# Performance work log

Measured on AMD Instinct MI355X. Metric: run time of the kernel, lower is better.

The kernel has to match this reference:

```python
import jax, jax.numpy as jnp
import numpy as np

HEADS = 8
DIM_HEAD = 64
BN_EPS = 1e-5

def setup_inputs() -> dict:
    key = jax.random.key(0)
    ks = jax.random.split(key, 6)
    B, N, D = 8, 1024, 512
    inner = HEADS * DIM_HEAD  # 512
    return {
        "x": jax.random.normal(ks[0], (B, N, D), dtype=jnp.float32),
        "w_qkv": jax.random.normal(ks[1], (D, 3 * inner), dtype=jnp.float32) * (D ** -0.5),
        "conv_w": jax.random.normal(ks[2], (HEADS, HEADS), dtype=jnp.float32) * (HEADS ** -0.5),
        "conv_b": jax.random.normal(ks[3], (HEADS,), dtype=jnp.float32) * 0.02,
        "bn_gamma": jnp.ones((HEADS,), dtype=jnp.float32),
        "bn_beta": jnp.zeros((HEADS,), dtype=jnp.float32),
        "w_out": jax.random.normal(ks[4], (inner, D), dtype=jnp.float32) * (inner ** -0.5),
        "b_out": jnp.zeros((D,), dtype=jnp.float32),
    }

def reference(x, w_qkv, conv_w, conv_b, bn_gamma, bn_beta, w_out, b_out):
    B, N, D = x.shape
    H, dh = HEADS, DIM_HEAD
    scale = dh ** -0.5
    qkv = x @ w_qkv  # [B, N, 3*H*dh]
    q, k, v = jnp.split(qkv, 3, axis=-1)
    # b n (h d) -> b h n d
    q = q.reshape(B, N, H, dh).transpose(0, 2, 1, 3)
    k = k.reshape(B, N, H, dh).transpose(0, 2, 1, 3)
    v = v.reshape(B, N, H, dh).transpose(0, 2, 1, 3)
    attn = jnp.einsum('bhnd,bhmd->bhnm', q, k) * scale
    attn = jax.nn.softmax(attn, axis=-1)
    # 1x1 conv across heads (channels = heads)
    attn = jnp.einsum('gh,bhnm->bgnm', conv_w, attn) + conv_b[None, :, None, None]
    # BatchNorm2d in training mode: batch stats over (B, N, N) per head, biased variance
    mean = attn.mean(axis=(0, 2, 3), keepdims=True)
    var = attn.var(axis=(0, 2, 3), keepdims=True)
    attn = (attn - mean) * jax.lax.rsqrt(var + BN_EPS)
    attn = attn * bn_gamma[None, :, None, None] + bn_beta[None, :, None, None]
    # reatten_scale = 1.0 (transform_scale=False)
    out = jnp.einsum('bhnm,bhmd->bhnd', attn, v)
    out = out.transpose(0, 2, 1, 3).reshape(B, N, H * dh)  # b h n d -> b n (h d)
    return out @ w_out + b_out
```

## Files before the change

kernel.cpp:

```cpp
#include <hip/hip_runtime.h>
#include <math.h>


#define Bz 8
#define Nn 1024
#define Dd 512
#define Hh 8
#define DH 64
#define INNER 512
#define QW 1536
#define SCALE 0.125f
#define BN_EPS 1e-5f

typedef _Float16 __f16;
typedef __f16 f16x8 __attribute__((ext_vector_type(8)));
typedef float f32x4 __attribute__((ext_vector_type(4)));

#define MFMA16(a, b, c) __builtin_amdgcn_mfma_f32_16x16x32_f16((a), (b), (c), 0, 0, 0)

__device__ __forceinline__ unsigned short f2h(float f) {
  union { __f16 h; unsigned short s; } v;
  v.h = (__f16)f;
  return v.s;
}
__device__ __forceinline__ float h2f(unsigned short s) {
  union { unsigned short s; __f16 h; } v;
  v.s = s;
  return (float)v.h;
}

#define WB_XB 0u
#define WB_QKV 8388608u
#define WB_VT 33554432u
#define WB_O1 41943040u
#define WB_O1BF 58720256u
#define WB_WQT 67108864u
#define WB_WOT 68681728u
#define WB_RINV 69206016u
#define WB_VSUM 69468160u
#define WB_STATS 69484544u
#define WB_AC 69484608u

__global__ __launch_bounds__(256) void k_xbf(const float* __restrict__ X,
                                             unsigned short* __restrict__ XB) {
  const size_t i = ((size_t)blockIdx.x * 256 + threadIdx.x) * 8;
  float4 f0 = *(const float4*)(X + i);
  float4 f1 = *(const float4*)(X + i + 4);
  unsigned short o[8] = {f2h(f0.x), f2h(f0.y), f2h(f0.z), f2h(f0.w),
                         f2h(f1.x), f2h(f1.y), f2h(f1.z), f2h(f1.w)};
  *(uint4*)(XB + i) = *(uint4*)o;
}

__global__ __launch_bounds__(256) void k_transpose(const float* __restrict__ src,
                                                   unsigned short* __restrict__ dst,
                                                   int R, int C) {
  __shared__ float tile[32][33];
  const int tc = blockIdx.x * 32, tr = blockIdx.y * 32;
  const int lx = threadIdx.x & 31, ly = threadIdx.x >> 5;
#pragma unroll
  for (int i = 0; i < 32; i += 8)
    tile[ly + i][lx] = src[(size_t)(tr + ly + i) * C + tc + lx];
  __syncthreads();
#pragma unroll
  for (int i = 0; i < 32; i += 8)
    dst[(size_t)(tc + ly + i) * R + tr + lx] = f2h(tile[lx][ly + i]);
}

__global__ __launch_bounds__(256) void k_qkv(const unsigned short* __restrict__ XB,
                                             const unsigned short* __restrict__ WQT,
                                             unsigned short* __restrict__ qkv,
                                             unsigned short* __restrict__ vT) {
  extern __shared__ char smem[];
  unsigned short(*sA)[40] = (unsigned short(*)[40])smem;
  unsigned short(*sB)[40] = (unsigned short(*)[40])(smem + 128 * 40 * 2);
  unsigned short* sEp = (unsigned short*)smem;
  const int t = threadIdx.x;
  const int col0 = blockIdx.x * 128;
  const int row0 = blockIdx.y * 128;
  const bool isqk = (col0 < 2 * INNER);
  const int l = t & 63, w = t >> 6;
  const int wm = (w & 1) * 64, wn = (w >> 1) * 64;
  const int lm = l & 15, lq = l >> 4;
  const int srow = t >> 1, skc = (t & 1) * 16;
  f32x4 acc[4][4] = {};
  for (int k0 = 0; k0 < Dd; k0 += 32) {
    {
      const unsigned short* src = XB + (size_t)(row0 + srow) * Dd + k0 + skc;
      *(uint4*)&sA[srow][skc] = *(const uint4*)src;
      *(uint4*)&sA[srow][skc + 8] = *(const uint4*)(src + 8);
    }
    {
      const unsigned short* srcB = WQT + (size_t)(col0 + srow) * Dd + k0 + skc;
      *(uint4*)&sB[srow][skc] = *(const uint4*)srcB;
      *(uint4*)&sB[srow][skc + 8] = *(const uint4*)(srcB + 8);
    }
    __syncthreads();
    f16x8 af[4], bfr[4];
#pragma unroll
    for (int i = 0; i < 4; i++) af[i] = *(const f16x8*)&sA[wm + 16 * i + lm][lq * 8];
#pragma unroll
    for (int j = 0; j < 4; j++) bfr[j] = *(const f16x8*)&sB[wn + 16 * j + lm][lq * 8];
    if (isqk) {
#pragma unroll
      for (int i = 0; i < 4; i++)
#pragma unroll
        for (int j = 0; j < 4; j++) acc[i][j] = MFMA16(bfr[i], af[j], acc[i][j]);
    } else {
#pragma unroll
      for (int i = 0; i < 4; i++)
#pragma unroll
        for (int j = 0; j < 4; j++) acc[i][j] = MFMA16(af[i], bfr[j], acc[i][j]);
    }
    __syncthreads();
  }
  if (isqk) {
#pragma unroll
    for (int jc = 0; jc < 4; jc++)
#pragma unroll
      for (int ir = 0; ir < 4; ir++) {
        unsigned short us[4];
#pragma unroll
        for (int r = 0; r < 4; r++) us[r] = f2h(acc[jc][ir][r]);
        *(uint2*)&sEp[(wm + 16 * ir + lm) * 136 + wn + 16 * jc + 4 * lq] = *(uint2*)us;
      }
    __syncthreads();
    const int row = t >> 1, half = t & 1;
    const unsigned short* src = &sEp[row * 136 + half * 64];
    unsigned short* dst = qkv + (size_t)(row0 + row) * QW + col0 + half * 64;
#pragma unroll
    for (int c = 0; c < 8; c++) *(uint4*)(dst + c * 8) = *(const uint4*)(src + c * 8);
  } else {
#pragma unroll
    for (int ir = 0; ir < 4; ir++)
#pragma unroll
      for (int jc = 0; jc < 4; jc++) {
        unsigned short us[4];
#pragma unroll
        for (int r = 0; r < 4; r++) us[r] = f2h(acc[ir][jc][r]);
        *(uint2*)&sEp[(wn + 16 * jc + lm) * 136 + wm + 16 * ir + 4 * lq] = *(uint2*)us;
      }
    __syncthreads();
    const int row = t >> 1, half = t & 1;
    const int gd = col0 - 2 * INNER + row;
    const int bq = row0 >> 10, mseq0 = row0 & 1023;
    const unsigned short* src = &sEp[row * 136 + half * 64];
    unsigned short* dst =
        vT + (((size_t)(bq * Hh + (gd >> 6)) * DH + (gd & 63)) << 10) + mseq0 + half * 64;
#pragma unroll
    for (int c = 0; c < 8; c++) *(uint4*)(dst + c * 8) = *(const uint4*)(src + c * 8);
  }
}

__global__ __launch_bounds__(256) void k_vsum(const unsigned short* __restrict__ vT,
                                              float* __restrict__ vsum) {
  const int bg = blockIdx.x;
  const int d = threadIdx.x >> 2, qq = threadIdx.x & 3;
  __shared__ float red[64][4];
  const unsigned short* p = vT + ((size_t)bg * DH + d) * Nn + qq * 256;
  float s = 0.f;
  for (int m = 0; m < 256; m += 4) {
    uint2 rr = *(const uint2*)(p + m);
    s += h2f((unsigned short)(rr.x & 0xffff)) + h2f((unsigned short)(rr.x >> 16)) +
         h2f((unsigned short)(rr.y & 0xffff)) + h2f((unsigned short)(rr.y >> 16));
  }
  red[d][qq] = s;
  __syncthreads();
  if (threadIdx.x < 64)
    vsum[(size_t)bg * DH + threadIdx.x] =
        red[threadIdx.x][0] + red[threadIdx.x][1] + red[threadIdx.x][2] + red[threadIdx.x][3];
}

__global__ __launch_bounds__(512, 2) void k_rsum(const unsigned short* __restrict__ qkv,
                                                 float* __restrict__ rinv) {
  const int b = blockIdx.x;
  const int n0 = blockIdx.y * 16;
  const int t = threadIdx.x;
  const int w = t >> 6, l = t & 63;
  const int lm = l & 15, lq = l >> 4;
  f16x8 qf[2];
  {
    const unsigned short* qp = qkv + (size_t)(b * Nn + n0 + lm) * QW + w * DH + lq * 8;
    qf[0] = *(const f16x8*)qp;
    qf[1] = *(const f16x8*)(qp + 32);
  }
  float psum[4] = {};
  for (int m0 = 0; m0 < Nn; m0 += 32) {
#pragma unroll
    for (int jm = 0; jm < 2; jm++) {
      const unsigned short* kp =
          qkv + (size_t)(b * Nn + m0 + 16 * jm + lm) * QW + INNER + w * DH + lq * 8;
      f16x8 k0 = *(const f16x8*)kp;
      f16x8 k1 = *(const f16x8*)(kp + 32);
      f32x4 lac = {};
      lac = MFMA16(qf[0], k0, lac);
      lac = MFMA16(qf[1], k1, lac);
#pragma unroll
      for (int r = 0; r < 4; r++) psum[r] += __expf(lac[r] * SCALE);
    }
  }
#pragma unroll
  for (int r = 0; r < 4; r++) {
    float s = psum[r];
    s += __shfl_xor(s, 1);
    s += __shfl_xor(s, 2);
    s += __shfl_xor(s, 4);
    s += __shfl_xor(s, 8);
    if (lm == 0) rinv[(size_t)(b * Hh + w) * Nn + n0 + lq * 4 + r] = 1.0f / s;
  }
}

__global__ __launch_bounds__(512, 2) void k_fuse(const unsigned short* __restrict__ qkv,
                                                 const unsigned short* __restrict__ vT,
                                                 const float* __restrict__ rinv,
                                                 const float* __restrict__ conv_w,
                                                 float* __restrict__ O1,
                                                 float* __restrict__ stats) {
  __shared__ __align__(16) unsigned short sS[8][16][36];
  __shared__ __align__(16) unsigned short sU[8][16][40];
  __shared__ float sRed[8][16];
  const int b = blockIdx.x;
  const int n0 = blockIdx.y * 16;
  const int t = threadIdx.x;
  const int w = t >> 6, l = t & 63;
  const int lm = l & 15, lq = l >> 4;
  const int mxn = t >> 5, mxm = t & 31;
  float cw[64];
#pragma unroll
  for (int i = 0; i < 64; i++) cw[i] = conv_w[i];
  f16x8 qf[2];
  {
    const unsigned short* qp = qkv + (size_t)(b * Nn + n0 + lm) * QW + w * DH + lq * 8;
    qf[0] = *(const f16x8*)qp;
    qf[1] = *(const f16x8*)(qp + 32);
  }
  float rv[4];
#pragma unroll
  for (int r = 0; r < 4; r++)
    rv[r] = rinv[(size_t)(b * Hh + w) * Nn + n0 + lq * 4 + r];
  f32x4 oacc[4] = {};
  float su[8] = {}, su2[8] = {};
  for (int m0 = 0; m0 < Nn; m0 += 32) {
    {
#pragma unroll
      for (int jm = 0; jm < 2; jm++) {
        const unsigned short* kp =
            qkv + (size_t)(b * Nn + m0 + 16 * jm + lm) * QW + INNER + w * DH + lq * 8;
        f16x8 k0 = *(const f16x8*)kp;
        f16x8 k1 = *(const f16x8*)(kp + 32);
        f32x4 lac = {};
        lac = MFMA16(qf[0], k0, lac);
        lac = MFMA16(qf[1], k1, lac);
#pragma unroll
        for (int r = 0; r < 4; r++)
          sS[w][lq * 4 + r][16 * jm + lm] = f2h(__expf(lac[r] * SCALE) * rv[r]);
      }
    }
    __syncthreads();
    {
      float sv[8];
#pragma unroll
      for (int h = 0; h < 8; h++) sv[h] = h2f(sS[h][mxn][mxm]);
#pragma unroll
      for (int g = 0; g < 8; g++) {
        float u = 0.f;
#pragma unroll
        for (int h = 0; h < 8; h++) u += cw[g * 8 + h] * sv[h];
        su[g] += u;
        su2[g] += u * u;
        sU[g][mxn][mxm] = f2h(u);
      }
    }
    __syncthreads();
    {
      f16x8 uf = *(const f16x8*)&sU[w][lm][lq * 8];
#pragma unroll
      for (int j = 0; j < 4; j++) {
        const unsigned short* vp =
            vT + (((size_t)(b * Hh + w) * DH + 16 * j + lm) << 10) + m0 + lq * 8;
        f16x8 vv = *(const f16x8*)vp;
        oacc[j] = MFMA16(uf, vv, oacc[j]);
      }
    }
  }
#pragma unroll
  for (int j = 0; j < 4; j++)
#pragma unroll
    for (int r = 0; r < 4; r++)
      O1[((size_t)(b * Hh + w) * Nn + n0 + lq * 4 + r) * DH + 16 * j + lm] = oacc[j][r];
#pragma unroll
  for (int g = 0; g < 8; g++) {
    float a = su[g], q = su2[g];
    for (int off = 32; off; off >>= 1) {
      a += __shfl_down(a, off);
      q += __shfl_down(q, off);
    }
    if (l == 0) {
      sRed[w][g] = a;
      sRed[w][8 + g] = q;
    }
  }
  __syncthreads();
  if (t < 16) {
    float s = 0.f;
#pragma unroll
    for (int ww = 0; ww < 8; ww++) s += sRed[ww][t];
    atomicAdd(&stats[t], s);
  }
}

__global__ void k_alpha(const float* __restrict__ stats, const float* __restrict__ bn_gamma,
                        const float* __restrict__ bn_beta, float* __restrict__ ac) {
  const int g = threadIdx.x;
  if (g < 8) {
    const float cnt = (float)Bz * (float)Nn * (float)Nn;
    float Eu = stats[g] / cnt;
    float Eu2 = stats[8 + g] / cnt;
    float inv = rsqrtf(Eu2 - Eu * Eu + BN_EPS);
    float alpha = bn_gamma[g] * inv;
    ac[g] = alpha;
    ac[8 + g] = bn_beta[g] - Eu * alpha;
  }
}

__global__ __launch_bounds__(256) void k_o1aff(const float* __restrict__ O1,
                                               const float* __restrict__ vsum,
                                               const float* __restrict__ ac,
                                               unsigned short* __restrict__ O1BF) {
  const size_t i4 = ((size_t)blockIdx.x * 256 + threadIdx.x) * 4;
  const int bg = (int)(i4 >> 16);
  const int g = bg & 7;
  const int d = (int)(i4 & 63);
  float4 a = *(const float4*)(O1 + i4);
  float4 v = *(const float4*)(vsum + (size_t)bg * DH + d);
  const float al = ac[g], cc = ac[8 + g];
  unsigned short o[4] = {f2h(al * a.x + cc * v.x), f2h(al * a.y + cc * v.y),
                         f2h(al * a.z + cc * v.z), f2h(al * a.w + cc * v.w)};
  *(uint2*)(O1BF + i4) = *(uint2*)o;
}

__global__ __launch_bounds__(256) void k_out(const unsigned short* __restrict__ O1BF,
                                             const unsigned short* __restrict__ WOT,
                                             const float* __restrict__ bout,
                                             float* __restrict__ out) {
  __shared__ unsigned short sA[128][40];
  __shared__ unsigned short sB[128][40];
  const int t = threadIdx.x;
  const int col0 = blockIdx.x * 128, row0 = blockIdx.y * 128;
  const int l = t & 63, w = t >> 6;
  const int wm = (w & 1) * 64, wn = (w >> 1) * 64;
  const int lm = l & 15, lq = l >> 4;
  const int srow = t >> 1, skc = (t & 1) * 16;
  const int b = row0 >> 10;
  const int nn = (row0 + srow) & 1023;
  f32x4 acc[4][4] = {};
  for (int k0 = 0; k0 < INNER; k0 += 32) {
    {
      const int k = k0 + skc;
      const int g = k >> 6, dd = k & 63;
      const unsigned short* src = O1BF + ((size_t)(b * Hh + g) * Nn + nn) * DH + dd;
      *(uint4*)&sA[srow][skc] = *(const uint4*)src;
      *(uint4*)&sA[srow][skc + 8] = *(const uint4*)(src + 8);
    }
    {
      const unsigned short* srcB = WOT + (size_t)(col0 + srow) * INNER + k0 + skc;
      *(uint4*)&sB[srow][skc] = *(const uint4*)srcB;
      *(uint4*)&sB[srow][skc + 8] = *(const uint4*)(srcB + 8);
    }
    __syncthreads();
    f16x8 af[4], bfr[4];
#pragma unroll
    for (int i = 0; i < 4; i++) af[i] = *(const f16x8*)&sA[wm + 16 * i + lm][lq * 8];
#pragma unroll
    for (int j = 0; j < 4; j++) bfr[j] = *(const f16x8*)&sB[wn + 16 * j + lm][lq * 8];
#pragma unroll
    for (int i = 0; i < 4; i++)
#pragma unroll
      for (int j = 0; j < 4; j++) acc[i][j] = MFMA16(af[i], bfr[j], acc[i][j]);
    __syncthreads();
  }
#pragma unroll
  for (int j = 0; j < 4; j++) {
    const int col = col0 + wn + 16 * j + lm;
    const float bo = bout[col];
#pragma unroll
    for (int i = 0; i < 4; i++) {
      const int rbase = row0 + wm + 16 * i + lq * 4;
#pragma unroll
      for (int r = 0; r < 4; r++) out[(size_t)(rbase + r) * Dd + col] = acc[i][j][r] + bo;
    }
  }
}

extern "C" void kernel_launch(void* const* d_in, const int* in_sizes, int n_in,
                              void* d_out, int out_size, void* d_ws, size_t ws_size,
                              hipStream_t stream) {
  const float* x = (const float*)d_in[0];
  const float* w_qkv = (const float*)d_in[1];
  const float* conv_w = (const float*)d_in[2];
  const float* bn_gamma = (const float*)d_in[4];
  const float* bn_beta = (const float*)d_in[5];
  const float* w_out = (const float*)d_in[6];
  const float* b_out = (const float*)d_in[7];
  char* ws = (char*)d_ws;
  unsigned short* XB = (unsigned short*)(ws + WB_XB);
  unsigned short* QKV = (unsigned short*)(ws + WB_QKV);
  unsigned short* VT = (unsigned short*)(ws + WB_VT);
  unsigned short* WQT = (unsigned short*)(ws + WB_WQT);
  unsigned short* WOT = (unsigned short*)(ws + WB_WOT);
  float* O1 = (float*)(ws + WB_O1);
  unsigned short* O1BF = (unsigned short*)(ws + WB_O1BF);
  float* RINV = (float*)(ws + WB_RINV);
  float* VSUM = (float*)(ws + WB_VSUM);
  float* STATS = (float*)(ws + WB_STATS);
  float* AC = (float*)(ws + WB_AC);

  hipMemsetAsync(STATS, 0, 64, stream);
  k_xbf<<<2048, 256, 0, stream>>>(x, XB);
  k_transpose<<<dim3(48, 16), 256, 0, stream>>>(w_qkv, WQT, 512, 1536);
  k_transpose<<<dim3(16, 16), 256, 0, stream>>>(w_out, WOT, 512, 512);
  k_qkv<<<dim3(12, 64), 256, 34816, stream>>>(XB, WQT, QKV, VT);
  k_vsum<<<64, 256, 0, stream>>>(VT, VSUM);
  k_rsum<<<dim3(8, 64), 512, 0, stream>>>(QKV, RINV);
  k_fuse<<<dim3(8, 64), 512, 0, stream>>>(QKV, VT, RINV, conv_w, O1, STATS);
  k_alpha<<<1, 64, 0, stream>>>(STATS, bn_gamma, bn_beta, AC);
  k_o1aff<<<4096, 256, 0, stream>>>(O1, VSUM, AC, O1BF);
  k_out<<<dim3(4, 64), 256, 0, stream>>>(O1BF, WOT, b_out, (float*)d_out);
}
```

Baseline: 337.6 us.

## Keep head-mixing conv in registers via transposed MFMA; split key range across blocks

The fused attention kernel now computes scores with K as the MFMA A operand, so each lane holds all 8 heads for the same query/key positions. This lets the 1x1 head-mixing conv happen entirely in registers, removing the shared-memory staging and both __syncthreads per tile. The key dimension is split into two halves across grid z, with partial outputs summed in k_o1aff. The BN mean is now computed analytically from the conv weights, since each softmax row sums to one, which drops the first-moment reduction. The row-sum kernel is restructured the same way. The costs are higher register pressure (16 Q fragments plus 64 accumulators), an extra output buffer, and more atomics on the stats.

```diff
diff --git a/kernel.cpp b/kernel.cpp
--- a/kernel.cpp
+++ b/kernel.cpp
@@ -14,9 +14,11 @@
 
 typedef _Float16 __f16;
 typedef __f16 f16x8 __attribute__((ext_vector_type(8)));
+typedef __f16 f16x4 __attribute__((ext_vector_type(4)));
 typedef float f32x4 __attribute__((ext_vector_type(4)));
 
 #define MFMA16(a, b, c) __builtin_amdgcn_mfma_f32_16x16x32_f16((a), (b), (c), 0, 0, 0)
+#define MFMA16K16(a, b, c) __builtin_amdgcn_mfma_f32_16x16x16f16((a), (b), (c), 0, 0, 0)
 
 __device__ __forceinline__ unsigned short f2h(float f) {
   union { __f16 h; unsigned short s; } v;
@@ -32,14 +34,15 @@
 #define WB_XB 0u
 #define WB_QKV 8388608u
 #define WB_VT 33554432u
-#define WB_O1 41943040u
-#define WB_O1BF 58720256u
-#define WB_WQT 67108864u
-#define WB_WOT 68681728u
-#define WB_RINV 69206016u
-#define WB_VSUM 69468160u
-#define WB_STATS 69484544u
-#define WB_AC 69484608u
+#define WB_O1A 41943040u
+#define WB_O1B 58720256u
+#define WB_O1BF 75497472u
+#define WB_WQT 83886080u
+#define WB_WOT 85458944u
+#define WB_RINV 85983232u
+#define WB_VSUM 86245376u
+#define WB_STATS 86261760u
+#define WB_AC 86261824u
 
 __global__ __launch_bounds__(256) void k_xbf(const float* __restrict__ X,
                                              unsigned short* __restrict__ XB) {
@@ -170,151 +173,150 @@
         red[threadIdx.x][0] + red[threadIdx.x][1] + red[threadIdx.x][2] + red[threadIdx.x][3];
 }
 
-__global__ __launch_bounds__(512, 2) void k_rsum(const unsigned short* __restrict__ qkv,
+__global__ __launch_bounds__(512, 4) void k_rsum(const unsigned short* __restrict__ qkv,
                                                  float* __restrict__ rinv) {
+  __shared__ float sRed[8][8][16];
   const int b = blockIdx.x;
   const int n0 = blockIdx.y * 16;
   const int t = threadIdx.x;
   const int w = t >> 6, l = t & 63;
   const int lm = l & 15, lq = l >> 4;
-  f16x8 qf[2];
-  {
-    const unsigned short* qp = qkv + (size_t)(b * Nn + n0 + lm) * QW + w * DH + lq * 8;
-    qf[0] = *(const f16x8*)qp;
-    qf[1] = *(const f16x8*)(qp + 32);
-  }
-  float psum[4] = {};
-  for (int m0 = 0; m0 < Nn; m0 += 32) {
-#pragma unroll
-    for (int jm = 0; jm < 2; jm++) {
-      const unsigned short* kp =
-          qkv + (size_t)(b * Nn + m0 + 16 * jm + lm) * QW + INNER + w * DH + lq * 8;
-      f16x8 k0 = *(const f16x8*)kp;
-      f16x8 k1 = *(const f16x8*)(kp + 32);
+  f16x8 qf[8][2];
+#pragma unroll
+  for (int h = 0; h < 8; h++) {
+    const unsigned short* qp = qkv + (size_t)(b * Nn + n0 + lm) * QW + h * DH + lq * 8;
+    qf[h][0] = *(const f16x8*)qp;
+    qf[h][1] = *(const f16x8*)(qp + 32);
+  }
+  float psum[8] = {};
+  for (int it = 0; it < 8; it++) {
+    const int m0 = w * 16 + it * 128;
+    const unsigned short* kbase = qkv + (size_t)(b * Nn + m0 + lm) * QW + INNER + lq * 8;
+#pragma unroll
+    for (int h = 0; h < 8; h++) {
+      f16x8 k0 = *(const f16x8*)(kbase + h * DH);
+      f16x8 k1 = *(const f16x8*)(kbase + h * DH + 32);
       f32x4 lac = {};
-      lac = MFMA16(qf[0], k0, lac);
-      lac = MFMA16(qf[1], k1, lac);
-#pragma unroll
-      for (int r = 0; r < 4; r++) psum[r] += __expf(lac[r] * SCALE);
-    }
-  }
-#pragma unroll
-  for (int r = 0; r < 4; r++) {
-    float s = psum[r];
-    s += __shfl_xor(s, 1);
-    s += __shfl_xor(s, 2);
-    s += __shfl_xor(s, 4);
-    s += __shfl_xor(s, 8);
-    if (lm == 0) rinv[(size_t)(b * Hh + w) * Nn + n0 + lq * 4 + r] = 1.0f / s;
-  }
-}
-
-__global__ __launch_bounds__(512, 2) void k_fuse(const unsigned short* __restrict__ qkv,
+      lac = MFMA16(k0, qf[h][0], lac);
+      lac = MFMA16(k1, qf[h][1], lac);
+#pragma unroll
+      for (int r = 0; r < 4; r++) psum[h] += __expf(lac[r] * SCALE);
+    }
+  }
+#pragma unroll
+  for (int h = 0; h < 8; h++) {
+    float p = psum[h];
+    p += __shfl_xor(p, 16);
+    p += __shfl_xor(p, 32);
+    if (lq == 0) sRed[w][h][lm] = p;
+  }
+  __syncthreads();
+  if (t < 128) {
+    const int h = t >> 4, n = t & 15;
+    float s = 0.f;
+#pragma unroll
+    for (int ww = 0; ww < 8; ww++) s += sRed[ww][h][n];
+    rinv[(size_t)(b * Hh + h) * Nn + n0 + n] = 1.0f / s;
+  }
+}
+
+__global__ __launch_bounds__(128, 2) void k_fuse(const unsigned short* __restrict__ qkv,
                                                  const unsigned short* __restrict__ vT,
                                                  const float* __restrict__ rinv,
                                                  const float* __restrict__ conv_w,
-                                                 float* __restrict__ O1,
+                                                 float* __restrict__ O1A,
+                                                 float* __restrict__ O1B,
                                                  float* __restrict__ stats) {
-  __shared__ __align__(16) unsigned short sS[8][16][36];
-  __shared__ __align__(16) unsigned short sU[8][16][40];
-  __shared__ float sRed[8][16];
   const int b = blockIdx.x;
   const int n0 = blockIdx.y * 16;
+  const int ms = blockIdx.z;
+  float* __restrict__ O1 = ms ? O1B : O1A;
   const int t = threadIdx.x;
-  const int w = t >> 6, l = t & 63;
-  const int lm = l & 15, lq = l >> 4;
-  const int mxn = t >> 5, mxm = t & 31;
-  float cw[64];
-#pragma unroll
-  for (int i = 0; i < 64; i++) cw[i] = conv_w[i];
-  f16x8 qf[2];
-  {
-    const unsigned short* qp = qkv + (size_t)(b * Nn + n0 + lm) * QW + w * DH + lq * 8;
-    qf[0] = *(const f16x8*)qp;
-    qf[1] = *(const f16x8*)(qp + 32);
-  }
-  float rv[4];
-#pragma unroll
-  for (int r = 0; r < 4; r++)
-    rv[r] = rinv[(size_t)(b * Hh + w) * Nn + n0 + lq * 4 + r];
-  f32x4 oacc[4] = {};
-  float su[8] = {}, su2[8] = {};
-  for (int m0 = 0; m0 < Nn; m0 += 32) {
-    {
-#pragma unroll
-      for (int jm = 0; jm < 2; jm++) {
-        const unsigned short* kp =
-            qkv + (size_t)(b * Nn + m0 + 16 * jm + lm) * QW + INNER + w * DH + lq * 8;
-        f16x8 k0 = *(const f16x8*)kp;
-        f16x8 k1 = *(const f16x8*)(kp + 32);
-        f32x4 lac = {};
-        lac = MFMA16(qf[0], k0, lac);
-        lac = MFMA16(qf[1], k1, lac);
-#pragma unroll
-        for (int r = 0; r < 4; r++)
-          sS[w][lq * 4 + r][16 * jm + lm] = f2h(__expf(lac[r] * SCALE) * rv[r]);
+  const int l = t & 63, lm = l & 15, lq = l >> 4;
+  const int ghu = __builtin_amdgcn_readfirstlane(t >> 6);
+  float cw[32];
+  if (ghu == 0) {
+#pragma unroll
+    for (int i = 0; i < 32; i++) cw[i] = conv_w[i];
+  } else {
+#pragma unroll
+    for (int i = 0; i < 32; i++) cw[i] = conv_w[32 + i];
+  }
+  float rv[8];
+#pragma unroll
+  for (int h = 0; h < 8; h++) rv[h] = rinv[(size_t)(b * Hh + h) * Nn + n0 + lm];
+  f16x8 qf[8][2];
+#pragma unroll
+  for (int h = 0; h < 8; h++) {
+    const unsigned short* qp = qkv + (size_t)(b * Nn + n0 + lm) * QW + h * DH + lq * 8;
+    qf[h][0] = *(const f16x8*)qp;
+    qf[h][1] = *(const f16x8*)(qp + 32);
+  }
+  f32x4 acc[4][4] = {};
+  float su2[4] = {};
+  for (int it = 0; it < 32; it++) {
+    const int m0 = ms * 512 + it * 16;
+    const unsigned short* kbase = qkv + (size_t)(b * Nn + m0 + lm) * QW + INNER + lq * 8;
+    float u[4][4] = {};
+#pragma unroll
+    for (int h = 0; h < 8; h++) {
+      f16x8 k0 = *(const f16x8*)(kbase + h * DH);
+      f16x8 k1 = *(const f16x8*)(kbase + h * DH + 32);
+      f32x4 lac = {};
+      lac = MFMA16(k0, qf[h][0], lac);
+      lac = MFMA16(k1, qf[h][1], lac);
+      float s[4];
+#pragma unroll
+      for (int r = 0; r < 4; r++) s[r] = __expf(lac[r] * SCALE) * rv[h];
+#pragma unroll
+      for (int gl = 0; gl < 4; gl++)
+#pragma unroll
+        for (int r = 0; r < 4; r++) u[gl][r] += cw[gl * 8 + h] * s[r];
+    }
+#pragma unroll
+    for (int gl = 0; gl < 4; gl++) {
+      su2[gl] += u[gl][0] * u[gl][0] + u[gl][1] * u[gl][1] + u[gl][2] * u[gl][2] +
+                 u[gl][3] * u[gl][3];
+      f16x4 up = {(__f16)u[gl][0], (__f16)u[gl][1], (__f16)u[gl][2], (__f16)u[gl][3]};
+      const int g = ghu * 4 + gl;
+      const unsigned short* vb =
+          vT + (((size_t)(b * Hh + g) * DH + lm) << 10) + m0 + lq * 4;
+#pragma unroll
+      for (int dt = 0; dt < 4; dt++) {
+        f16x4 vf = *(const f16x4*)(vb + ((size_t)dt << 14));
+        acc[gl][dt] = MFMA16K16(up, vf, acc[gl][dt]);
       }
     }
-    __syncthreads();
-    {
-      float sv[8];
-#pragma unroll
-      for (int h = 0; h < 8; h++) sv[h] = h2f(sS[h][mxn][mxm]);
-#pragma unroll
-      for (int g = 0; g < 8; g++) {
-        float u = 0.f;
-#pragma unroll
-        for (int h = 0; h < 8; h++) u += cw[g * 8 + h] * sv[h];
-        su[g] += u;
-        su2[g] += u * u;
-        sU[g][mxn][mxm] = f2h(u);
-      }
-    }
-    __syncthreads();
-    {
-      f16x8 uf = *(const f16x8*)&sU[w][lm][lq * 8];
-#pragma unroll
-      for (int j = 0; j < 4; j++) {
-        const unsigned short* vp =
-            vT + (((size_t)(b * Hh + w) * DH + 16 * j + lm) << 10) + m0 + lq * 8;
-        f16x8 vv = *(const f16x8*)vp;
-        oacc[j] = MFMA16(uf, vv, oacc[j]);
-      }
-    }
-  }
-#pragma unroll
-  for (int j = 0; j < 4; j++)
-#pragma unroll
-    for (int r = 0; r < 4; r++)
-      O1[((size_t)(b * Hh + w) * Nn + n0 + lq * 4 + r) * DH + 16 * j + lm] = oacc[j][r];
-#pragma unroll
-  for (int g = 0; g < 8; g++) {
-    float a = su[g], q = su2[g];
-    for (int off = 32; off; off >>= 1) {
-      a += __shfl_down(a, off);
-      q += __shfl_down(q, off);
-    }
-    if (l == 0) {
-      sRed[w][g] = a;
-      sRed[w][8 + g] = q;
-    }
-  }
-  __syncthreads();
-  if (t < 16) {
-    float s = 0.f;
-#pragma unroll
-    for (int ww = 0; ww < 8; ww++) s += sRed[ww][t];
-    atomicAdd(&stats[t], s);
-  }
-}
-
-__global__ void k_alpha(const float* __restrict__ stats, const float* __restrict__ bn_gamma,
+  }
+#pragma unroll
+  for (int gl = 0; gl < 4; gl++) {
+    const int g = ghu * 4 + gl;
+#pragma unroll
+    for (int dt = 0; dt < 4; dt++)
+#pragma unroll
+      for (int r = 0; r < 4; r++)
+        O1[((size_t)(b * Hh + g) * Nn + n0 + lq * 4 + r) * DH + dt * 16 + lm] =
+            acc[gl][dt][r];
+  }
+#pragma unroll
+  for (int gl = 0; gl < 4; gl++) {
+    float q = su2[gl];
+    for (int off = 32; off; off >>= 1) q += __shfl_down(q, off);
+    if (l == 0) atomicAdd(&stats[ghu * 4 + gl], q);
+  }
+}
+
+__global__ void k_alpha(const float* __restrict__ stats, const float* __restrict__ conv_w,
+                        const float* __restrict__ bn_gamma,
                         const float* __restrict__ bn_beta, float* __restrict__ ac) {
   const int g = threadIdx.x;
   if (g < 8) {
+    float csum = 0.f;
+#pragma unroll
+    for (int h = 0; h < 8; h++) csum += conv_w[g * 8 + h];
+    const float Eu = csum / (float)Nn;
     const float cnt = (float)Bz * (float)Nn * (float)Nn;
-    float Eu = stats[g] / cnt;
-    float Eu2 = stats[8 + g] / cnt;
+    float Eu2 = stats[g] / cnt;
     float inv = rsqrtf(Eu2 - Eu * Eu + BN_EPS);
     float alpha = bn_gamma[g] * inv;
     ac[g] = alpha;
@@ -322,7 +324,8 @@
   }
 }
 
-__global__ __launch_bounds__(256) void k_o1aff(const float* __restrict__ O1,
+__global__ __launch_bounds__(256) void k_o1aff(const float* __restrict__ O1A,
+                                               const float* __restrict__ O1B,
                                                const float* __restrict__ vsum,
                                                const float* __restrict__ ac,
                                                unsigned short* __restrict__ O1BF) {
@@ -330,11 +333,12 @@
   const int bg = (int)(i4 >> 16);
   const int g = bg & 7;
   const int d = (int)(i4 & 63);
-  float4 a = *(const float4*)(O1 + i4);
+  float4 a = *(const float4*)(O1A + i4);
+  float4 bb = *(const float4*)(O1B + i4);
   float4 v = *(const float4*)(vsum + (size_t)bg * DH + d);
   const float al = ac[g], cc = ac[8 + g];
-  unsigned short o[4] = {f2h(al * a.x + cc * v.x), f2h(al * a.y + cc * v.y),
-                         f2h(al * a.z + cc * v.z), f2h(al * a.w + cc * v.w)};
+  unsigned short o[4] = {f2h(al * (a.x + bb.x) + cc * v.x), f2h(al * (a.y + bb.y) + cc * v.y),
+                         f2h(al * (a.z + bb.z) + cc * v.z), f2h(al * (a.w + bb.w) + cc * v.w)};
   *(uint2*)(O1BF + i4) = *(uint2*)o;
 }
 
@@ -407,7 +411,8 @@
   unsigned short* VT = (unsigned short*)(ws + WB_VT);
   unsigned short* WQT = (unsigned short*)(ws + WB_WQT);
   unsigned short* WOT = (unsigned short*)(ws + WB_WOT);
-  float* O1 = (float*)(ws + WB_O1);
+  float* O1Ap = (float*)(ws + WB_O1A);
+  float* O1Bp = (float*)(ws + WB_O1B);
   unsigned short* O1BF = (unsigned short*)(ws + WB_O1BF);
   float* RINV = (float*)(ws + WB_RINV);
   float* VSUM = (float*)(ws + WB_VSUM);
@@ -421,8 +426,8 @@
   k_qkv<<<dim3(12, 64), 256, 34816, stream>>>(XB, WQT, QKV, VT);
   k_vsum<<<64, 256, 0, stream>>>(VT, VSUM);
   k_rsum<<<dim3(8, 64), 512, 0, stream>>>(QKV, RINV);
-  k_fuse<<<dim3(8, 64), 512, 0, stream>>>(QKV, VT, RINV, conv_w, O1, STATS);
-  k_alpha<<<1, 64, 0, stream>>>(STATS, bn_gamma, bn_beta, AC);
-  k_o1aff<<<4096, 256, 0, stream>>>(O1, VSUM, AC, O1BF);
+  k_fuse<<<dim3(8, 64, 2), 128, 0, stream>>>(QKV, VT, RINV, conv_w, O1Ap, O1Bp, STATS);
+  k_alpha<<<1, 64, 0, stream>>>(STATS, conv_w, bn_gamma, bn_beta, AC);
+  k_o1aff<<<4096, 256, 0, stream>>>(O1Ap, O1Bp, VSUM, AC, O1BF);
   k_out<<<dim3(4, 64), 256, 0, stream>>>(O1BF, WOT, b_out, (float*)d_out);
 }
```

Result: slower. 576.5 us (+70.8%).

## Widen fused attention tile, derive BN mean analytically, fold affine into output GEMM

Applied to the files above, without the earlier changes.

The fused attention kernel now processes 128 keys per iteration instead of 32, which cuts barriers per key. It uses transposed MFMA operands so softmax values are written to shared memory as packed vectors. The BN mean is computed analytically from the conv weight row sums, since softmax rows sum to one, so only the sum of squares is accumulated. The per-element affine pass is removed: the intermediate is stored in fp16 and the BN affine plus vsum correction is applied while loading the A tile of the output GEMM. This trades an extra kernel and an fp32 round trip for fp16 precision in the intermediate and more register and LDS pressure.

```diff
diff --git a/kernel.cpp b/kernel.cpp
--- a/kernel.cpp
+++ b/kernel.cpp
@@ -32,14 +32,13 @@
 #define WB_XB 0u
 #define WB_QKV 8388608u
 #define WB_VT 33554432u
-#define WB_O1 41943040u
-#define WB_O1BF 58720256u
-#define WB_WQT 67108864u
-#define WB_WOT 68681728u
-#define WB_RINV 69206016u
-#define WB_VSUM 69468160u
-#define WB_STATS 69484544u
-#define WB_AC 69484608u
+#define WB_O1H 41943040u
+#define WB_WQT 50331648u
+#define WB_WOT 51904512u
+#define WB_RINV 52428800u
+#define WB_VSUM 52690944u
+#define WB_STATS 52707328u
+#define WB_AC 52707392u
 
 __global__ __launch_bounds__(256) void k_xbf(const float* __restrict__ X,
                                              unsigned short* __restrict__ XB) {
@@ -184,6 +183,7 @@
     qf[1] = *(const f16x8*)(qp + 32);
   }
   float psum[4] = {};
+#pragma unroll 2
   for (int m0 = 0; m0 < Nn; m0 += 32) {
 #pragma unroll
     for (int jm = 0; jm < 2; jm++) {
@@ -209,21 +209,22 @@
   }
 }
 
-__global__ __launch_bounds__(512, 2) void k_fuse(const unsigned short* __restrict__ qkv,
-                                                 const unsigned short* __restrict__ vT,
-                                                 const float* __restrict__ rinv,
-                                                 const float* __restrict__ conv_w,
-                                                 float* __restrict__ O1,
-                                                 float* __restrict__ stats) {
-  __shared__ __align__(16) unsigned short sS[8][16][36];
-  __shared__ __align__(16) unsigned short sU[8][16][40];
-  __shared__ float sRed[8][16];
+__global__ __launch_bounds__(512, 2) void k_fuse2(const unsigned short* __restrict__ qkv,
+                                                  const unsigned short* __restrict__ vT,
+                                                  const float* __restrict__ rinv,
+                                                  const float* __restrict__ conv_w,
+                                                  unsigned short* __restrict__ O1H,
+                                                  float* __restrict__ stats) {
+  __shared__ unsigned short sS[8][16][132];
+  __shared__ unsigned short sU[8][16][132];
+  __shared__ float sRedS[8][8];
   const int b = blockIdx.x;
   const int n0 = blockIdx.y * 16;
   const int t = threadIdx.x;
   const int w = t >> 6, l = t & 63;
   const int lm = l & 15, lq = l >> 4;
-  const int mxn = t >> 5, mxm = t & 31;
+  const int mn = t >> 5;
+  const int mj = t & 31;
   float cw[64];
 #pragma unroll
   for (int i = 0; i < 64; i++) cw[i] = conv_w[i];
@@ -233,88 +234,97 @@
     qf[0] = *(const f16x8*)qp;
     qf[1] = *(const f16x8*)(qp + 32);
   }
-  float rv[4];
-#pragma unroll
-  for (int r = 0; r < 4; r++)
-    rv[r] = rinv[(size_t)(b * Hh + w) * Nn + n0 + lq * 4 + r];
-  f32x4 oacc[4] = {};
-  float su[8] = {}, su2[8] = {};
-  for (int m0 = 0; m0 < Nn; m0 += 32) {
+  const float rv = rinv[(size_t)(b * Hh + w) * Nn + n0 + lm];
+  f32x4 acc[4] = {};
+  float su2[8] = {};
+  for (int it = 0; it < 8; it++) {
+    const int m0 = it * 128;
+#pragma unroll
+    for (int jm = 0; jm < 8; jm++) {
+      const unsigned short* kp =
+          qkv + (size_t)(b * Nn + m0 + jm * 16 + lm) * QW + INNER + w * DH + lq * 8;
+      f16x8 k0 = *(const f16x8*)kp;
+      f16x8 k1 = *(const f16x8*)(kp + 32);
+      f32x4 lac = {};
+      lac = MFMA16(k0, qf[0], lac);
+      lac = MFMA16(k1, qf[1], lac);
+      unsigned short us[4];
+#pragma unroll
+      for (int r = 0; r < 4; r++) us[r] = f2h(__expf(lac[r] * SCALE) * rv);
+      *(uint2*)&sS[w][lm][jm * 16 + lq * 4] = *(uint2*)us;
+    }
+    __syncthreads();
     {
-#pragma unroll
-      for (int jm = 0; jm < 2; jm++) {
-        const unsigned short* kp =
-            qkv + (size_t)(b * Nn + m0 + 16 * jm + lm) * QW + INNER + w * DH + lq * 8;
-        f16x8 k0 = *(const f16x8*)kp;
-        f16x8 k1 = *(const f16x8*)(kp + 32);
-        f32x4 lac = {};
-        lac = MFMA16(qf[0], k0, lac);
-        lac = MFMA16(qf[1], k1, lac);
-#pragma unroll
-        for (int r = 0; r < 4; r++)
-          sS[w][lq * 4 + r][16 * jm + lm] = f2h(__expf(lac[r] * SCALE) * rv[r]);
-      }
-    }
-    __syncthreads();
-    {
-      float sv[8];
-#pragma unroll
-      for (int h = 0; h < 8; h++) sv[h] = h2f(sS[h][mxn][mxm]);
+      float f[8][4];
+#pragma unroll
+      for (int h = 0; h < 8; h++) {
+        uint2 pk = *(const uint2*)&sS[h][mn][mj * 4];
+        f[h][0] = h2f((unsigned short)(pk.x & 0xffff));
+        f[h][1] = h2f((unsigned short)(pk.x >> 16));
+        f[h][2] = h2f((unsigned short)(pk.y & 0xffff));
+        f[h][3] = h2f((unsigned short)(pk.y >> 16));
+      }
 #pragma unroll
       for (int g = 0; g < 8; g++) {
-        float u = 0.f;
-#pragma unroll
-        for (int h = 0; h < 8; h++) u += cw[g * 8 + h] * sv[h];
-        su[g] += u;
-        su2[g] += u * u;
-        sU[g][mxn][mxm] = f2h(u);
-      }
-    }
-    __syncthreads();
-    {
-      f16x8 uf = *(const f16x8*)&sU[w][lm][lq * 8];
-#pragma unroll
-      for (int j = 0; j < 4; j++) {
+        float u0 = 0.f, u1 = 0.f, u2 = 0.f, u3 = 0.f;
+#pragma unroll
+        for (int h = 0; h < 8; h++) {
+          const float c = cw[g * 8 + h];
+          u0 += c * f[h][0];
+          u1 += c * f[h][1];
+          u2 += c * f[h][2];
+          u3 += c * f[h][3];
+        }
+        su2[g] += u0 * u0 + u1 * u1 + u2 * u2 + u3 * u3;
+        unsigned short us[4] = {f2h(u0), f2h(u1), f2h(u2), f2h(u3)};
+        *(uint2*)&sU[g][mn][mj * 4] = *(uint2*)us;
+      }
+    }
+    __syncthreads();
+#pragma unroll
+    for (int ks = 0; ks < 4; ks++) {
+      f16x8 uf = *(const f16x8*)&sU[w][lm][ks * 32 + lq * 8];
+#pragma unroll
+      for (int dt = 0; dt < 4; dt++) {
         const unsigned short* vp =
-            vT + (((size_t)(b * Hh + w) * DH + 16 * j + lm) << 10) + m0 + lq * 8;
-        f16x8 vv = *(const f16x8*)vp;
-        oacc[j] = MFMA16(uf, vv, oacc[j]);
-      }
-    }
-  }
-#pragma unroll
-  for (int j = 0; j < 4; j++)
+            vT + (((size_t)(b * Hh + w) * DH + dt * 16 + lm) << 10) + m0 + ks * 32 + lq * 8;
+        f16x8 vf = *(const f16x8*)vp;
+        acc[dt] = MFMA16(uf, vf, acc[dt]);
+      }
+    }
+  }
+#pragma unroll
+  for (int dt = 0; dt < 4; dt++)
 #pragma unroll
     for (int r = 0; r < 4; r++)
-      O1[((size_t)(b * Hh + w) * Nn + n0 + lq * 4 + r) * DH + 16 * j + lm] = oacc[j][r];
+      O1H[((size_t)(b * Hh + w) * Nn + n0 + lq * 4 + r) * DH + dt * 16 + lm] =
+          f2h(acc[dt][r]);
 #pragma unroll
   for (int g = 0; g < 8; g++) {
-    float a = su[g], q = su2[g];
-    for (int off = 32; off; off >>= 1) {
-      a += __shfl_down(a, off);
-      q += __shfl_down(q, off);
-    }
-    if (l == 0) {
-      sRed[w][g] = a;
-      sRed[w][8 + g] = q;
-    }
+    float q = su2[g];
+    for (int off = 32; off; off >>= 1) q += __shfl_down(q, off);
+    if (l == 0) sRedS[w][g] = q;
   }
   __syncthreads();
-  if (t < 16) {
+  if (t < 8) {
     float s = 0.f;
 #pragma unroll
-    for (int ww = 0; ww < 8; ww++) s += sRed[ww][t];
+    for (int ww = 0; ww < 8; ww++) s += sRedS[ww][t];
     atomicAdd(&stats[t], s);
   }
 }
 
-__global__ void k_alpha(const float* __restrict__ stats, const float* __restrict__ bn_gamma,
+__global__ void k_alpha(const float* __restrict__ stats, const float* __restrict__ conv_w,
+                        const float* __restrict__ bn_gamma,
                         const float* __restrict__ bn_beta, float* __restrict__ ac) {
   const int g = threadIdx.x;
   if (g < 8) {
+    float csum = 0.f;
+#pragma unroll
+    for (int h = 0; h < 8; h++) csum += conv_w[g * 8 + h];
+    const float Eu = csum / (float)Nn;
     const float cnt = (float)Bz * (float)Nn * (float)Nn;
-    float Eu = stats[g] / cnt;
-    float Eu2 = stats[8 + g] / cnt;
+    float Eu2 = stats[g] / cnt;
     float inv = rsqrtf(Eu2 - Eu * Eu + BN_EPS);
     float alpha = bn_gamma[g] * inv;
     ac[g] = alpha;
@@ -322,29 +332,17 @@
   }
 }
 
-__global__ __launch_bounds__(256) void k_o1aff(const float* __restrict__ O1,
-                                               const float* __restrict__ vsum,
-                                               const float* __restrict__ ac,
-                                               unsigned short* __restrict__ O1BF) {
-  const size_t i4 = ((size_t)blockIdx.x * 256 + threadIdx.x) * 4;
-  const int bg = (int)(i4 >> 16);
-  const int g = bg & 7;
-  const int d = (int)(i4 & 63);
-  float4 a = *(const float4*)(O1 + i4);
-  float4 v = *(const float4*)(vsum + (size_t)bg * DH + d);
-  const float al = ac[g], cc = ac[8 + g];
-  unsigned short o[4] = {f2h(al * a.x + cc * v.x), f2h(al * a.y + cc * v.y),
-                         f2h(al * a.z + cc * v.z), f2h(al * a.w + cc * v.w)};
-  *(uint2*)(O1BF + i4) = *(uint2*)o;
-}
-
-__global__ __launch_bounds__(256) void k_out(const unsigned short* __restrict__ O1BF,
+__global__ __launch_bounds__(256) void k_out(const unsigned short* __restrict__ O1H,
+                                             const float* __restrict__ vsum,
+                                             const float* __restrict__ ac,
                                              const unsigned short* __restrict__ WOT,
                                              const float* __restrict__ bout,
                                              float* __restrict__ out) {
   __shared__ unsigned short sA[128][40];
   __shared__ unsigned short sB[128][40];
+  __shared__ float sAl[16];
   const int t = threadIdx.x;
+  if (t < 16) sAl[t] = ac[t];
   const int col0 = blockIdx.x * 128, row0 = blockIdx.y * 128;
   const int l = t & 63, w = t >> 6;
   const int wm = (w & 1) * 64, wn = (w >> 1) * 64;
@@ -353,13 +351,33 @@
   const int b = row0 >> 10;
   const int nn = (row0 + srow) & 1023;
   f32x4 acc[4][4] = {};
+  __syncthreads();
   for (int k0 = 0; k0 < INNER; k0 += 32) {
     {
       const int k = k0 + skc;
       const int g = k >> 6, dd = k & 63;
-      const unsigned short* src = O1BF + ((size_t)(b * Hh + g) * Nn + nn) * DH + dd;
-      *(uint4*)&sA[srow][skc] = *(const uint4*)src;
-      *(uint4*)&sA[srow][skc + 8] = *(const uint4*)(src + 8);
+      const float al = sAl[g], cc = sAl[8 + g];
+      const unsigned short* op = O1H + ((size_t)(b * Hh + g) * Nn + nn) * DH + dd;
+      const float* vp = vsum + (size_t)(b * Hh + g) * DH + dd;
+      uint4 o0 = *(const uint4*)op;
+      uint4 o1 = *(const uint4*)(op + 8);
+      unsigned short tmp[16];
+      const unsigned* ow = (const unsigned*)&o0;
+#pragma unroll
+      for (int c = 0; c < 4; c++) {
+        float v0 = vp[c * 2], v1 = vp[c * 2 + 1];
+        tmp[c * 2] = f2h(al * h2f((unsigned short)(ow[c] & 0xffff)) + cc * v0);
+        tmp[c * 2 + 1] = f2h(al * h2f((unsigned short)(ow[c] >> 16)) + cc * v1);
+      }
+      const unsigned* ow1 = (const unsigned*)&o1;
+#pragma unroll
+      for (int c = 0; c < 4; c++) {
+        float v0 = vp[8 + c * 2], v1 = vp[8 + c * 2 + 1];
+        tmp[8 + c * 2] = f2h(al * h2f((unsigned short)(ow1[c] & 0xffff)) + cc * v0);
+        tmp[8 + c * 2 + 1] = f2h(al * h2f((unsigned short)(ow1[c] >> 16)) + cc * v1);
+      }
+      *(uint4*)&sA[srow][skc] = *(uint4*)tmp;
+      *(uint4*)&sA[srow][skc + 8] = *(uint4*)(tmp + 8);
     }
     {
       const unsigned short* srcB = WOT + (size_t)(col0 + srow) * INNER + k0 + skc;
@@ -405,10 +423,9 @@
   unsigned short* XB = (unsigned short*)(ws + WB_XB);
   unsigned short* QKV = (unsigned short*)(ws + WB_QKV);
   unsigned short* VT = (unsigned short*)(ws + WB_VT);
+  unsigned short* O1H = (unsigned short*)(ws + WB_O1H);
   unsigned short* WQT = (unsigned short*)(ws + WB_WQT);
   unsigned short* WOT = (unsigned short*)(ws + WB_WOT);
-  float* O1 = (float*)(ws + WB_O1);
-  unsigned short* O1BF = (unsigned short*)(ws + WB_O1BF);
   float* RINV = (float*)(ws + WB_RINV);
   float* VSUM = (float*)(ws + WB_VSUM);
   float* STATS = (float*)(ws + WB_STATS);
@@ -421,8 +438,7 @@
   k_qkv<<<dim3(12, 64), 256, 34816, stream>>>(XB, WQT, QKV, VT);
   k_vsum<<<64, 256, 0, stream>>>(VT, VSUM);
   k_rsum<<<dim3(8, 64), 512, 0, stream>>>(QKV, RINV);
-  k_fuse<<<dim3(8, 64), 512, 0, stream>>>(QKV, VT, RINV, conv_w, O1, STATS);
-  k_alpha<<<1, 64, 0, stream>>>(STATS, bn_gamma, bn_beta, AC);
-  k_o1aff<<<4096, 256, 0, stream>>>(O1, VSUM, AC, O1BF);
-  k_out<<<dim3(4, 64), 256, 0, stream>>>(O1BF, WOT, b_out, (float*)d_out);
-}
+  k_fuse2<<<dim3(8, 64), 512, 0, stream>>>(QKV, VT, RINV, conv_w, O1H, STATS);
+  k_alpha<<<1, 64, 0, stream>>>(STATS, conv_w, bn_gamma, bn_beta, AC);
+  k_out<<<dim3(4, 64), 256, 0, stream>>>(O1H, VSUM, AC, WOT, b_out, (float*)d_out);
+}
```

Measured after the change: 336.5 us. Within noise of the previous version (-0.3%).
